# Kernel optimization log

Hardware: AMD Instinct MI355X
Metric: run time of the kernel (lower is better)

The kernel has to match this reference:

```python
import jax, jax.numpy as jnp
import numpy as np

B, L = 16, 54            # dialogues, utterances per dialogue
NDIM = 512; H = 512; NS = 2
T = B * L                # 864 utterances
N = 3 * T                # 2592 nodes (l,a,v per utterance)
NE = B * (L + 3)         # 912 hyperedges (3 modality + L utterance per dialogue)
NNZ = 6 * T              # 5184 incidence entries
E = B * 3 * L * (L - 1)  # 137376 directed intra-modality edges
NUM_L = 3; NUM_K = 4
EPS = 1e-8


def _build_indices():
    rng = np.random.default_rng(0)
    spk = rng.integers(0, NS, size=(B, L))
    # qmask [L, B, NS] one-hot of speakers (matches torch argmax path)
    qmask = np.eye(NS, dtype=np.float32)[spk].transpose(1, 0, 2)
    ar = np.arange(L)
    i1, i2, ht = [], [], []
    for d in range(B):
        base = d * 3 * L
        nl = base + ar; na = nl + L; nv = nl + 2 * L
        # 3 modality hyperedges then L per-utterance (l,a,v) hyperedges
        i1 += [nl, na, nv, np.stack([nl, na, nv], 1).reshape(-1)]
        eb = d * (L + 3)
        i2 += [np.repeat(eb + np.arange(3), L), np.repeat(eb + 3 + ar, 3)]
        ht += [np.ones(L, np.int64), np.zeros(3, np.int64)]
    hyperedge_index = np.stack([np.concatenate(i1), np.concatenate(i2)]).astype(np.int64)
    hyperedge_type = np.concatenate(ht)
    # full permutation edges within each modality of each dialogue
    s0 = np.repeat(ar, L); d0 = np.tile(ar, L)
    m = s0 != d0; s0, d0 = s0[m], d0[m]
    src, dst, et = [], [], []
    for d in range(B):
        same = (spk[d][s0] == spk[d][d0]).astype(np.int64)
        for mm in range(3):
            off = d * 3 * L + mm * L
            src.append(s0 + off); dst.append(d0 + off); et.append(same)
    edge_index = np.stack([np.concatenate(src), np.concatenate(dst)]).astype(np.int64)
    edge_type = np.concatenate(et)
    return qmask, hyperedge_index, hyperedge_type, edge_index, edge_type


def setup_inputs() -> dict:
    key = jax.random.key(0)
    ks = jax.random.split(key, 16)
    qmask, hei, het, ei, et = _build_indices()
    n = lambda k, s: jax.random.normal(k, s, dtype=jnp.float32)
    inp = {
        'a': n(ks[0], (T, NDIM)), 'v': n(ks[1], (T, NDIM)), 'l': n(ks[2], (T, NDIM)),
        'qmask': jnp.asarray(qmask),
        'spk_emb': n(ks[3], (NS, NDIM)) * 0.05,
        'fc1_W': n(ks[4], (NDIM, H)) * 0.05, 'fc1_b': jnp.zeros((H,), jnp.float32),
        'he_weight': jnp.ones((NE,), jnp.float32),
        'ew_weight': jnp.ones((NNZ,), jnp.float32),
        'he_attr1': jax.random.uniform(ks[5], (H,), dtype=jnp.float32),
        'he_attr2': jax.random.uniform(ks[6], (H,), dtype=jnp.float32),
        'hc_W': n(ks[7], (NUM_L, H, H)) * 0.05, 'hc_b': jnp.zeros((NUM_L, H), jnp.float32),
        'm3_W0': n(ks[8], (NUM_K, H, H)) * 0.05,
        'm3_W1': n(ks[9], (NUM_K, H, H)) * 0.05,
        'm3_Wself': n(ks[10], (NUM_K, H, H)) * 0.05,
        'm3_b': jnp.zeros((NUM_K, H), jnp.float32),
        'hyperedge_index': jnp.asarray(hei), 'hyperedge_type': jnp.asarray(het),
        'edge_index': jnp.asarray(ei), 'edge_type': jnp.asarray(et),
    }
    return inp


def reference(a, v, l, qmask, spk_emb, fc1_W, fc1_b, he_weight, ew_weight,
              he_attr1, he_attr2, hc_W, hc_b, m3_W0, m3_W1, m3_Wself, m3_b,
              hyperedge_index, hyperedge_type, edge_index, edge_type):
    seg = jax.ops.segment_sum
    # speaker embedding added to text modality (equal dia_len -> simple transpose)
    qm = qmask.transpose(1, 0, 2).reshape(T, NS)
    l = l + spk_emb[jnp.argmax(qm, axis=-1)]
    # per-dialogue node order: [l_d ; a_d ; v_d]
    feats = jnp.concatenate([l.reshape(B, L, NDIM), a.reshape(B, L, NDIM),
                             v.reshape(B, L, NDIM)], axis=1).reshape(N, NDIM)
    x1 = feats @ fc1_W + fc1_b
    node_i, edge_i = hyperedge_index[0], hyperedge_index[1]
    tfl = hyperedge_type.astype(x1.dtype)[:, None]
    edge_attr = he_attr1[None, :] * tfl + he_attr2[None, :] * (1.0 - tfl)  # [NE,H]
    out = x1
    for ll in range(NUM_L):  # hypergraph conv: gather->edge agg->scatter->linear
        de = seg(ew_weight, edge_i, num_segments=NE)
        e = seg(ew_weight[:, None] * out[node_i], edge_i, num_segments=NE)
        e = e / (de + EPS)[:, None] + edge_attr
        c = he_weight[edge_i]
        dn = seg(c, node_i, num_segments=N)
        agg = seg(c[:, None] * e[edge_i], node_i, num_segments=N) / (dn + EPS)[:, None]
        out = jax.nn.relu(agg @ hc_W[ll] + hc_b[ll])
    src, dst = edge_index[0], edge_index[1]
    same_spk = (edge_type == 1)[:, None]
    deg = seg(jnp.ones_like(dst, dtype=x1.dtype), dst, num_segments=N)
    gnn_out = x1
    denoise = jnp.float32(0.0)
    for kk in range(NUM_K):  # 2-relation RGCN-style denoise layer
        h0 = gnn_out @ m3_W0[kk]
        h1 = gnn_out @ m3_W1[kk]
        msg = jnp.where(same_spk, h1[src], h0[src])
        agg = seg(msg, dst, num_segments=N) / (deg + EPS)[:, None]
        f = jax.nn.relu(agg + gnn_out @ m3_Wself[kk] + m3_b[kk])
        denoise = jnp.mean(f * f)
        gnn_out = gnn_out + f
    return out + gnn_out, denoise
```

## Files before the change

### kernel.cpp

```cpp
#include <hip/hip_runtime.h>

typedef unsigned short ushort_t;
typedef __attribute__((ext_vector_type(4))) float f32x4;
typedef __attribute__((ext_vector_type(8))) short s16x8;
typedef __attribute__((ext_vector_type(8))) unsigned short u16x8;

#define NB 16
#define NL 54
#define NT (NB*NL)
#define NNODE (3*NT)
#define NEDGE 912
#define MATSZ (512*512)

__device__ __forceinline__ ushort_t f2b(float f){
  union {unsigned int i; float f;} x; x.f = f;
  unsigned int r = (x.i + 0x7fffu + ((x.i>>16)&1u))>>16;
  return (ushort_t)r;
}

__device__ __forceinline__ void async_copy16(const ushort_t* g, ushort_t* l){
  __builtin_amdgcn_global_load_lds((const __attribute__((address_space(1))) void*)g,
                                   (__attribute__((address_space(3))) void*)l, 16, 0, 0);
}

__global__ __launch_bounds__(256) void transpose_weights(
    const float* __restrict__ fc1, const float* __restrict__ hc,
    const float* __restrict__ m0, const float* __restrict__ m1,
    const float* __restrict__ ms, ushort_t* __restrict__ WT,
    float* __restrict__ acc, unsigned int* __restrict__ counter)
{
  if (blockIdx.x==0 && blockIdx.y==0 && blockIdx.z==0 && threadIdx.x==0){
    *acc = 0.0f; *counter = 0u;
  }
  int w = blockIdx.z;
  const float* src = (w==0) ? fc1
                   : (w<4)  ? hc + (size_t)(w-1)*MATSZ
                   : (w<8)  ? m0 + (size_t)(w-4)*MATSZ
                   : (w<12) ? m1 + (size_t)(w-8)*MATSZ
                            : ms + (size_t)(w-12)*MATSZ;
  ushort_t* dst = WT + (size_t)w*MATSZ;
  __shared__ float tile[64][65];
  int r0 = blockIdx.x*64, c0 = blockIdx.y*64;
  #pragma unroll
  for (int j=0;j<16;j++){
    int idx = j*256 + threadIdx.x;
    int r = idx>>6, c = idx&63;
    tile[r][c] = src[(size_t)(r0+r)*512 + c0 + c];
  }
  __syncthreads();
  #pragma unroll
  for (int j=0;j<16;j++){
    int idx = j*256 + threadIdx.x;
    int r = idx>>6, c = idx&63;
    dst[(size_t)(c0+r)*512 + r0 + c] = f2b(tile[c][r]);
  }
}

template<int AMODE, bool RELU>
__global__ __launch_bounds__(256) void gemm_kernel(
    const float* __restrict__ Afp, const float* __restrict__ Ebuf,
    const float* __restrict__ inA, const float* __restrict__ inV,
    const float* __restrict__ inL, const float* __restrict__ qmask,
    const float* __restrict__ spk_emb, const float* __restrict__ he_w,
    const ushort_t* __restrict__ WT, const float* __restrict__ bias,
    float* __restrict__ C0, float* __restrict__ C1, float* __restrict__ C2,
    int layer)
{
  const int tid = threadIdx.x;
  const int wave = tid>>6, lane = tid&63;
  const int ml = lane&15, quad = lane>>4;
  const int wr = wave>>1, wc = wave&1;
  int row0 = blockIdx.x*64, col0 = blockIdx.y*128;
  int M = NNODE, cst = 512, cbase = 0;
  const ushort_t* Wsel = WT; float* Cout = C0; const float* bsel = bias;
  const float* Asrc = Afp;
  if (AMODE==2){
    int z = blockIdx.z;
    if (z==0){ Wsel = WT + (size_t)(8+layer)*MATSZ; Cout = C0; bsel = nullptr; }
    else if (z==1){ Wsel = WT + (size_t)(12+layer)*MATSZ; Cout = C1; bsel = bias + layer*512; }
    else {
      if (blockIdx.x >= 4) return;
      int colh = blockIdx.x & 1;
      row0 = (blockIdx.x>>1)*64;
      Wsel = WT + (size_t)(4 + colh*4 + layer)*MATSZ;
      Cout = C2; bsel = nullptr; M = 96; cst = 1024; cbase = colh*512;
      Asrc = Ebuf;
    }
  }

  __shared__ __align__(16) ushort_t As[64][80];
  __shared__ __align__(16) ushort_t Bs[128*64];

  const int ar = tid>>3, ac8 = (tid&7)*8;
  const float *sr0=nullptr,*sr1=nullptr,*sp0=nullptr,*sp1=nullptr;
  const float *e10=nullptr,*e20=nullptr,*e11=nullptr,*e21=nullptr;
  float c10=0.f,c20=0.f,c11=0.f,c21=0.f;
  const float *g0=nullptr,*g1=nullptr;
  {
    int n0 = row0+ar;     if (n0 > M-1) n0 = M-1;
    int n1 = row0+ar+32;  if (n1 > M-1) n1 = M-1;
    if (AMODE==0){
      int d=n0/162, rm=n0-d*162, m=rm/54, i=rm-m*54, t=d*54+i;
      sr0 = ((m==0)? inL : (m==1)? inA : inV) + (size_t)t*512;
      if (m==0) sp0 = spk_emb + ((qmask[(i*16+d)*2+1]>qmask[(i*16+d)*2])?512:0);
      d=n1/162; rm=n1-d*162; m=rm/54; i=rm-m*54; t=d*54+i;
      sr1 = ((m==0)? inL : (m==1)? inA : inV) + (size_t)t*512;
      if (m==0) sp1 = spk_emb + ((qmask[(i*16+d)*2+1]>qmask[(i*16+d)*2])?512:0);
    } else if (AMODE==1){
      int d=n0/162, rm=n0-d*162, m=rm/54, i=rm-m*54;
      int em=d*57+m, eu=d*57+3+i;
      float w1=he_w[em], w2=he_w[eu], inv=1.0f/(w1+w2+1e-8f);
      c10=w1*inv; c20=w2*inv; e10=Ebuf+(size_t)em*512; e20=Ebuf+(size_t)eu*512;
      d=n1/162; rm=n1-d*162; m=rm/54; i=rm-m*54;
      em=d*57+m; eu=d*57+3+i;
      w1=he_w[em]; w2=he_w[eu]; inv=1.0f/(w1+w2+1e-8f);
      c11=w1*inv; c21=w2*inv; e11=Ebuf+(size_t)em*512; e21=Ebuf+(size_t)eu*512;
    } else {
      g0 = Asrc + (size_t)n0*512;
      g1 = Asrc + (size_t)n1*512;
    }
  }

  f32x4 acc[2][4];
  #pragma unroll
  for (int mi=0;mi<2;mi++)
    #pragma unroll
    for (int j=0;j<4;j++) acc[mi][j] = (f32x4){0.f,0.f,0.f,0.f};

  const int lr = lane>>3;
  const int lchunk = lane&7;
  const int bswz = (lchunk ^ lr)*8;

  for (int kk=0; kk<512; kk+=64){
    u16x8 av0, av1;
    if (AMODE==0){
      f32x4 xa=*(const f32x4*)(sr0+kk+ac8), xb=*(const f32x4*)(sr0+kk+ac8+4);
      if (sp0){
        f32x4 sa=*(const f32x4*)(sp0+kk+ac8), sb=*(const f32x4*)(sp0+kk+ac8+4);
        #pragma unroll
        for(int j=0;j<4;j++){ xa[j]+=sa[j]; xb[j]+=sb[j]; }
      }
      #pragma unroll
      for(int j=0;j<4;j++){ av0[j]=f2b(xa[j]); av0[4+j]=f2b(xb[j]); }
      xa=*(const f32x4*)(sr1+kk+ac8); xb=*(const f32x4*)(sr1+kk+ac8+4);
      if (sp1){
        f32x4 sa=*(const f32x4*)(sp1+kk+ac8), sb=*(const f32x4*)(sp1+kk+ac8+4);
        #pragma unroll
        for(int j=0;j<4;j++){ xa[j]+=sa[j]; xb[j]+=sb[j]; }
      }
      #pragma unroll
      for(int j=0;j<4;j++){ av1[j]=f2b(xa[j]); av1[4+j]=f2b(xb[j]); }
    } else if (AMODE==1){
      f32x4 xa=*(const f32x4*)(e10+kk+ac8), xb=*(const f32x4*)(e10+kk+ac8+4);
      f32x4 ya=*(const f32x4*)(e20+kk+ac8), yb=*(const f32x4*)(e20+kk+ac8+4);
      #pragma unroll
      for(int j=0;j<4;j++){ av0[j]=f2b(c10*xa[j]+c20*ya[j]); av0[4+j]=f2b(c10*xb[j]+c20*yb[j]); }
      xa=*(const f32x4*)(e11+kk+ac8); xb=*(const f32x4*)(e11+kk+ac8+4);
      ya=*(const f32x4*)(e21+kk+ac8); yb=*(const f32x4*)(e21+kk+ac8+4);
      #pragma unroll
      for(int j=0;j<4;j++){ av1[j]=f2b(c11*xa[j]+c21*ya[j]); av1[4+j]=f2b(c11*xb[j]+c21*yb[j]); }
    } else {
      f32x4 xa=*(const f32x4*)(g0+kk+ac8), xb=*(const f32x4*)(g0+kk+ac8+4);
      #pragma unroll
      for(int j=0;j<4;j++){ av0[j]=f2b(xa[j]); av0[4+j]=f2b(xb[j]); }
      xa=*(const f32x4*)(g1+kk+ac8); xb=*(const f32x4*)(g1+kk+ac8+4);
      #pragma unroll
      for(int j=0;j<4;j++){ av1[j]=f2b(xa[j]); av1[4+j]=f2b(xb[j]); }
    }
    *(u16x8*)&As[ar][ac8]    = av0;
    *(u16x8*)&As[ar+32][ac8] = av1;

    #pragma unroll
    for (int rep=0; rep<4; rep++){
      int bn0 = wave*32 + rep*8;
      const ushort_t* src = Wsel + (size_t)(col0 + bn0 + lr)*512 + kk + bswz;
      async_copy16(src, &Bs[bn0*64]);
    }
    __syncthreads();

    #pragma unroll
    for (int kh=0; kh<2; kh++){
      s16x8 a0 = *(const s16x8*)&As[wr*32 + ml][kh*32 + quad*8];
      s16x8 a1 = *(const s16x8*)&As[wr*32 + 16 + ml][kh*32 + quad*8];
      s16x8 b[4];
      #pragma unroll
      for (int j=0;j<4;j++){
        int bn = wc*64 + j*16 + ml;
        b[j] = *(const s16x8*)&Bs[bn*64 + (((kh*4+quad) ^ (bn&7))<<3)];
      }
      #pragma unroll
      for (int j=0;j<4;j++){
        acc[0][j] = __builtin_amdgcn_mfma_f32_16x16x32_bf16(a0,b[j],acc[0][j],0,0,0);
        acc[1][j] = __builtin_amdgcn_mfma_f32_16x16x32_bf16(a1,b[j],acc[1][j],0,0,0);
      }
    }
    __syncthreads();
  }

  #pragma unroll
  for (int j=0;j<4;j++){
    int wcol = col0 + wc*64 + j*16 + ml;
    float bv = bsel ? bsel[wcol] : 0.f;
    int c = cbase + wcol;
    #pragma unroll
    for (int mi=0;mi<2;mi++){
      int rb = row0 + wr*32 + mi*16 + quad*4;
      f32x4 a = acc[mi][j];
      #pragma unroll
      for (int r=0;r<4;r++){
        int rr = rb + r;
        if (rr < M){
          float v = a[r] + bv;
          if (RELU) v = fmaxf(v, 0.f);
          Cout[(size_t)rr*cst + c] = v;
        }
      }
    }
  }
}

__global__ __launch_bounds__(256) void edge_kernel(const float* __restrict__ X,
    const float* __restrict__ ew, const int* __restrict__ het,
    const float* __restrict__ at1, const float* __restrict__ at2,
    float* __restrict__ E)
{
  int e = blockIdx.x;
  int d = e/57, r = e - d*57;
  int col = threadIdx.x*2;
  float sx=0.f, sy=0.f, de=0.f;
  if (r < 3){
    int nnz0 = d*324 + r*54;
    const float* row = X + ((size_t)(d*162 + r*54))*512 + col;
    for (int i=0;i<54;i++){
      float w = ew[nnz0+i];
      float2 x = *(const float2*)row;
      sx += w*x.x; sy += w*x.y; de += w;
      row += 512;
    }
  } else {
    int i = r-3;
    int nnz0 = d*324 + 162 + i*3;
    #pragma unroll
    for (int m=0;m<3;m++){
      float w = ew[nnz0+m];
      const float* row = X + ((size_t)(d*162 + m*54 + i))*512 + col;
      float2 x = *(const float2*)row;
      sx += w*x.x; sy += w*x.y; de += w;
    }
  }
  float invde = 1.0f/(de + 1e-8f);
  const float* at = het[e] ? at1 : at2;
  float2 o;
  o.x = sx*invde + at[col];
  o.y = sy*invde + at[col+1];
  *(float2*)(E + (size_t)e*512 + col) = o;
}

__global__ __launch_bounds__(256) void gsum_kernel(const float* __restrict__ X,
    const float* __restrict__ qmask, float* __restrict__ Gsum)
{
  int g = blockIdx.x, d = g/3;
  int col = blockIdx.y*256 + threadIdx.x;
  __shared__ unsigned char spks[54];
  if (threadIdx.x < 54){
    int i = threadIdx.x;
    spks[i] = qmask[(i*16+d)*2+1] > qmask[(i*16+d)*2];
  }
  __syncthreads();
  size_t base = (size_t)g*54*512 + col;
  float s0=0.f, s1=0.f;
  for (int i=0;i<54;i++){
    float x = X[base + (size_t)i*512];
    if (spks[i]) s1 += x; else s0 += x;
  }
  Gsum[(size_t)(g*2)*512 + col]   = s0;
  Gsum[(size_t)(g*2+1)*512 + col] = s1;
}

template<bool LAST>
__global__ __launch_bounds__(256) void sf_kernel(
    const float* __restrict__ Gin, const float* __restrict__ H1,
    const float* __restrict__ HS, const float* __restrict__ Sp,
    const float* __restrict__ qmask, float* __restrict__ Gout,
    float* __restrict__ Gsum, const float* __restrict__ OUThg,
    float* __restrict__ dout, float* __restrict__ acc,
    unsigned int* __restrict__ counter)
{
  int g = blockIdx.x, d = g/3;
  int col = blockIdx.y*256 + threadIdx.x;
  __shared__ unsigned char spks[54];
  if (threadIdx.x < 54){
    int i = threadIdx.x;
    spks[i] = qmask[(i*16+d)*2+1] > qmask[(i*16+d)*2];
  }
  __syncthreads();
  const float* r0 = Sp + (size_t)(g*2)*1024;
  const float* r1 = Sp + (size_t)(g*2+1)*1024;
  float S1_0 = r0[512+col];
  float S1_1 = r1[512+col];
  float S0_0 = r1[col];
  float S0_1 = r0[col];
  const float inv = 1.0f/(53.0f + 1e-8f);
  size_t base = (size_t)g*54*512 + col;
  float gs0=0.f, gs1=0.f, sumsq=0.f;
  for (int i=0;i<54;i++){
    size_t off = base + (size_t)i*512;
    int sp = spks[i];
    float S1 = sp ? S1_1 : S1_0;
    float S0 = sp ? S0_1 : S0_0;
    float h1 = H1[off], hs = HS[off], gi = Gin[off];
    float f = fmaxf((S1 - h1 + S0)*inv + hs, 0.f);
    float gn = gi + f;
    Gout[off] = gn;
    if (sp) gs1 += gn; else gs0 += gn;
    if (LAST){
      sumsq += f*f;
      dout[off] = OUThg[off] + gn;
    }
  }
  Gsum[(size_t)(g*2)*512 + col]   = gs0;
  Gsum[(size_t)(g*2+1)*512 + col] = gs1;
  if (LAST){
    __shared__ float red[256];
    red[threadIdx.x] = sumsq;
    __syncthreads();
    #pragma unroll
    for (int s=128; s>0; s>>=1){
      if (threadIdx.x < s) red[threadIdx.x] += red[threadIdx.x+s];
      __syncthreads();
    }
    if (threadIdx.x == 0){
      atomicAdd(acc, red[0]);
      __threadfence();
      unsigned int old = atomicAdd(counter, 1u);
      if (old == 95u){
        float tot = atomicAdd(acc, 0.0f);
        dout[(size_t)NNODE*512] = tot * (1.0f/1327104.0f);
      }
    }
  }
}

extern "C" void kernel_launch(void* const* d_in, const int* in_sizes, int n_in,
                              void* d_out, int out_size, void* d_ws, size_t ws_size,
                              hipStream_t stream)
{
  const float* A_in   = (const float*)d_in[0];
  const float* V_in   = (const float*)d_in[1];
  const float* L_in   = (const float*)d_in[2];
  const float* qmask  = (const float*)d_in[3];
  const float* spk    = (const float*)d_in[4];
  const float* fc1_W  = (const float*)d_in[5];
  const float* fc1_b  = (const float*)d_in[6];
  const float* he_w   = (const float*)d_in[7];
  const float* ew_w   = (const float*)d_in[8];
  const float* attr1  = (const float*)d_in[9];
  const float* attr2  = (const float*)d_in[10];
  const float* hc_W   = (const float*)d_in[11];
  const float* hc_b   = (const float*)d_in[12];
  const float* m3_W0  = (const float*)d_in[13];
  const float* m3_W1  = (const float*)d_in[14];
  const float* m3_Ws  = (const float*)d_in[15];
  const float* m3_b   = (const float*)d_in[16];
  const int*   het    = (const int*)d_in[18];
  float* dout = (float*)d_out;

  char* ws = (char*)d_ws;
  ushort_t* WT = (ushort_t*)ws;
  float* X1   = (float*)(ws + (size_t)16*MATSZ*2);
  float* OUT  = X1  + (size_t)NNODE*512;
  float* H1   = OUT + (size_t)NNODE*512;
  float* HS   = H1  + (size_t)NNODE*512;
  float* G    = HS  + (size_t)NNODE*512;
  float* EB   = G   + (size_t)NNODE*512;
  float* Gsum = EB  + (size_t)NEDGE*512;
  float* Sp   = Gsum + 96*512;
  float* acc  = Sp  + 96*1024;
  unsigned int* counter = (unsigned int*)(acc + 1);

  transpose_weights<<<dim3(8,8,16),256,0,stream>>>(fc1_W, hc_W, m3_W0, m3_W1,
                                                   m3_Ws, WT, acc, counter);

  gemm_kernel<0,false><<<dim3(41,4,1),256,0,stream>>>(
      nullptr, nullptr, A_in, V_in, L_in, qmask, spk, nullptr,
      WT, fc1_b, X1, nullptr, nullptr, 0);

  gsum_kernel<<<dim3(48,2),256,0,stream>>>(X1, qmask, Gsum);

  const float* src = X1;
  for (int ll=0; ll<3; ll++){
    edge_kernel<<<NEDGE,256,0,stream>>>(src, ew_w, het, attr1, attr2, EB);
    gemm_kernel<1,true><<<dim3(41,4,1),256,0,stream>>>(
        nullptr, EB, nullptr, nullptr, nullptr, nullptr, nullptr, he_w,
        WT + (size_t)(1+ll)*MATSZ, hc_b + (size_t)ll*512, OUT, nullptr, nullptr, 0);
    src = OUT;
  }

  for (int kk=0; kk<4; kk++){
    const float* gin = (kk==0) ? X1 : G;
    gemm_kernel<2,false><<<dim3(41,4,3),256,0,stream>>>(
        gin, Gsum, nullptr, nullptr, nullptr, nullptr, nullptr, nullptr,
        WT, m3_b, H1, HS, Sp, kk);
    if (kk<3)
      sf_kernel<false><<<dim3(48,2),256,0,stream>>>(
          gin, H1, HS, Sp, qmask, G, Gsum, nullptr, nullptr, acc, counter);
    else
      sf_kernel<true><<<dim3(48,2),256,0,stream>>>(
          gin, H1, HS, Sp, qmask, G, Gsum, OUT, dout, acc, counter);
  }

  (void)in_sizes; (void)n_in; (void)out_size; (void)ws_size;
}
```

Measured before the change: 311.3 us.

## Fuse hypergraph and RGCN layers into paired multi-role kernels with folded weights

Restructures the pipeline into alternating ka/kb kernels. Each launch runs the hypergraph edge aggregation, its GEMM, the self/speaker-sum GEMMs and the RGCN update side by side in separate block ranges, which cuts the launch count from about 15 to 10. The per-node h1 term is removed algebraically by folding -W1/53 into the self weight during preprocessing, so the H1 GEMM disappears. The GEMM now stages a full 32x512 A tile in LDS and reads B directly from global memory rather than through an async LDS copy. In exchange it relies on the fixed all-pairs edge structure, uses ping-pong buffers, and bf16 rounding of the folded weights may shift numerics slightly.

```diff
diff --git a/kernel.cpp b/kernel.cpp
--- a/kernel.cpp
+++ b/kernel.cpp
@@ -5,12 +5,9 @@
 typedef __attribute__((ext_vector_type(8))) short s16x8;
 typedef __attribute__((ext_vector_type(8))) unsigned short u16x8;
 
-#define NB 16
-#define NL 54
-#define NT (NB*NL)
-#define NNODE (3*NT)
-#define NEDGE 912
+#define NNODE 2592
 #define MATSZ (512*512)
+#define INV53 (1.0f/(53.0f + 1e-8f))
 
 __device__ __forceinline__ ushort_t f2b(float f){
   union {unsigned int i; float f;} x; x.f = f;
@@ -18,34 +15,31 @@
   return (ushort_t)r;
 }
 
-__device__ __forceinline__ void async_copy16(const ushort_t* g, ushort_t* l){
-  __builtin_amdgcn_global_load_lds((const __attribute__((address_space(1))) void*)g,
-                                   (__attribute__((address_space(3))) void*)l, 16, 0, 0);
-}
-
-__global__ __launch_bounds__(256) void transpose_weights(
+__global__ __launch_bounds__(256) void prep_kernel(
     const float* __restrict__ fc1, const float* __restrict__ hc,
     const float* __restrict__ m0, const float* __restrict__ m1,
     const float* __restrict__ ms, ushort_t* __restrict__ WT,
     float* __restrict__ acc, unsigned int* __restrict__ counter)
 {
-  if (blockIdx.x==0 && blockIdx.y==0 && blockIdx.z==0 && threadIdx.x==0){
-    *acc = 0.0f; *counter = 0u;
-  }
-  int w = blockIdx.z;
+  if (blockIdx.x==0 && threadIdx.x==0){ *acc = 0.f; *counter = 0u; }
+  __shared__ float tile[64][65];
+  int w = blockIdx.x>>6, t = blockIdx.x&63, bx = t>>3, by = t&7;
   const float* src = (w==0) ? fc1
                    : (w<4)  ? hc + (size_t)(w-1)*MATSZ
                    : (w<8)  ? m0 + (size_t)(w-4)*MATSZ
                    : (w<12) ? m1 + (size_t)(w-8)*MATSZ
                             : ms + (size_t)(w-12)*MATSZ;
+  const float* src2 = (w>=12) ? m1 + (size_t)(w-12)*MATSZ : nullptr;
   ushort_t* dst = WT + (size_t)w*MATSZ;
-  __shared__ float tile[64][65];
-  int r0 = blockIdx.x*64, c0 = blockIdx.y*64;
+  int r0 = bx*64, c0 = by*64;
   #pragma unroll
   for (int j=0;j<16;j++){
     int idx = j*256 + threadIdx.x;
     int r = idx>>6, c = idx&63;
-    tile[r][c] = src[(size_t)(r0+r)*512 + c0 + c];
+    size_t off = (size_t)(r0+r)*512 + c0 + c;
+    float v = src[off];
+    if (w>=12) v -= INV53 * src2[off];
+    tile[r][c] = v;
   }
   __syncthreads();
   #pragma unroll
@@ -56,286 +50,330 @@
   }
 }
 
-template<int AMODE, bool RELU>
-__global__ __launch_bounds__(256) void gemm_kernel(
-    const float* __restrict__ Afp, const float* __restrict__ Ebuf,
-    const float* __restrict__ inA, const float* __restrict__ inV,
-    const float* __restrict__ inL, const float* __restrict__ qmask,
-    const float* __restrict__ spk_emb, const float* __restrict__ he_w,
-    const ushort_t* __restrict__ WT, const float* __restrict__ bias,
-    float* __restrict__ C0, float* __restrict__ C1, float* __restrict__ C2,
-    int layer)
+__device__ __forceinline__ void gemm32(const ushort_t* As,
+    const ushort_t* W, int col0, f32x4 acc[2][2])
 {
   const int tid = threadIdx.x;
   const int wave = tid>>6, lane = tid&63;
   const int ml = lane&15, quad = lane>>4;
-  const int wr = wave>>1, wc = wave&1;
-  int row0 = blockIdx.x*64, col0 = blockIdx.y*128;
-  int M = NNODE, cst = 512, cbase = 0;
-  const ushort_t* Wsel = WT; float* Cout = C0; const float* bsel = bias;
-  const float* Asrc = Afp;
-  if (AMODE==2){
-    int z = blockIdx.z;
-    if (z==0){ Wsel = WT + (size_t)(8+layer)*MATSZ; Cout = C0; bsel = nullptr; }
-    else if (z==1){ Wsel = WT + (size_t)(12+layer)*MATSZ; Cout = C1; bsel = bias + layer*512; }
-    else {
-      if (blockIdx.x >= 4) return;
-      int colh = blockIdx.x & 1;
-      row0 = (blockIdx.x>>1)*64;
-      Wsel = WT + (size_t)(4 + colh*4 + layer)*MATSZ;
-      Cout = C2; bsel = nullptr; M = 96; cst = 1024; cbase = colh*512;
-      Asrc = Ebuf;
-    }
-  }
-
-  __shared__ __align__(16) ushort_t As[64][80];
-  __shared__ __align__(16) ushort_t Bs[128*64];
-
-  const int ar = tid>>3, ac8 = (tid&7)*8;
-  const float *sr0=nullptr,*sr1=nullptr,*sp0=nullptr,*sp1=nullptr;
-  const float *e10=nullptr,*e20=nullptr,*e11=nullptr,*e21=nullptr;
-  float c10=0.f,c20=0.f,c11=0.f,c21=0.f;
-  const float *g0=nullptr,*g1=nullptr;
+  #pragma unroll
+  for (int mf=0;mf<2;mf++)
+    #pragma unroll
+    for (int nf=0;nf<2;nf++) acc[mf][nf] = (f32x4){0.f,0.f,0.f,0.f};
+
+  const ushort_t* bw0 = W + (size_t)(col0 + wave*32 + ml)*512 + quad*8;
+  const ushort_t* bw1 = bw0 + (size_t)16*512;
+  const int rsw = ml&7;
+  #pragma unroll
+  for (int ks=0; ks<16; ks++){
+    const int chunk = ks*4 + quad;
+    const int abase = (chunk>>3)*64 + (((chunk&7) ^ rsw)<<3);
+    s16x8 a0 = *(const s16x8*)&As[(size_t)ml*512 + abase];
+    s16x8 a1 = *(const s16x8*)&As[(size_t)(16+ml)*512 + abase];
+    s16x8 b0 = *(const s16x8*)(bw0 + ks*32);
+    s16x8 b1 = *(const s16x8*)(bw1 + ks*32);
+    acc[0][0] = __builtin_amdgcn_mfma_f32_16x16x32_bf16(a0,b0,acc[0][0],0,0,0);
+    acc[0][1] = __builtin_amdgcn_mfma_f32_16x16x32_bf16(a0,b1,acc[0][1],0,0,0);
+    acc[1][0] = __builtin_amdgcn_mfma_f32_16x16x32_bf16(a1,b0,acc[1][0],0,0,0);
+    acc[1][1] = __builtin_amdgcn_mfma_f32_16x16x32_bf16(a1,b1,acc[1][1],0,0,0);
+  }
+}
+
+__global__ __launch_bounds__(256) void fc1_kernel(
+    const float* __restrict__ A_in, const float* __restrict__ V_in,
+    const float* __restrict__ L_in, const float* __restrict__ qmask,
+    const float* __restrict__ spk, const ushort_t* __restrict__ WT,
+    const float* __restrict__ fc1_b, float* __restrict__ X1)
+{
+  __shared__ __align__(16) ushort_t As[32*512];
+  const int b = blockIdx.x, tid = threadIdx.x;
+  const int r0 = (b>>2)*32, col0 = (b&3)*128;
   {
-    int n0 = row0+ar;     if (n0 > M-1) n0 = M-1;
-    int n1 = row0+ar+32;  if (n1 > M-1) n1 = M-1;
-    if (AMODE==0){
-      int d=n0/162, rm=n0-d*162, m=rm/54, i=rm-m*54, t=d*54+i;
-      sr0 = ((m==0)? inL : (m==1)? inA : inV) + (size_t)t*512;
-      if (m==0) sp0 = spk_emb + ((qmask[(i*16+d)*2+1]>qmask[(i*16+d)*2])?512:0);
-      d=n1/162; rm=n1-d*162; m=rm/54; i=rm-m*54; t=d*54+i;
-      sr1 = ((m==0)? inL : (m==1)? inA : inV) + (size_t)t*512;
-      if (m==0) sp1 = spk_emb + ((qmask[(i*16+d)*2+1]>qmask[(i*16+d)*2])?512:0);
-    } else if (AMODE==1){
-      int d=n0/162, rm=n0-d*162, m=rm/54, i=rm-m*54;
-      int em=d*57+m, eu=d*57+3+i;
-      float w1=he_w[em], w2=he_w[eu], inv=1.0f/(w1+w2+1e-8f);
-      c10=w1*inv; c20=w2*inv; e10=Ebuf+(size_t)em*512; e20=Ebuf+(size_t)eu*512;
-      d=n1/162; rm=n1-d*162; m=rm/54; i=rm-m*54;
-      em=d*57+m; eu=d*57+3+i;
-      w1=he_w[em]; w2=he_w[eu]; inv=1.0f/(w1+w2+1e-8f);
-      c11=w1*inv; c21=w2*inv; e11=Ebuf+(size_t)em*512; e21=Ebuf+(size_t)eu*512;
+    int row = tid>>3, seg = tid&7, gr = r0+row;
+    int d = gr/162, rm = gr-d*162, m = rm/54, i = rm-m*54, t = d*54+i;
+    const float* pa = ((m==0)?L_in:(m==1)?A_in:V_in) + (size_t)t*512 + seg*64;
+    const float* pb = pa;
+    bool hassp = (m==0);
+    if (hassp){
+      int sp = qmask[(i*16+d)*2+1] > qmask[(i*16+d)*2];
+      pb = spk + sp*512 + seg*64;
+    }
+    int rsw = row&7;
+    ushort_t* dstA = &As[row*512 + seg*64];
+    #pragma unroll
+    for (int j=0;j<8;j++){
+      f32x4 xa = *(const f32x4*)(pa+j*8), xb = *(const f32x4*)(pa+j*8+4);
+      if (hassp){
+        f32x4 ya = *(const f32x4*)(pb+j*8), yb = *(const f32x4*)(pb+j*8+4);
+        #pragma unroll
+        for (int jj=0;jj<4;jj++){ xa[jj]+=ya[jj]; xb[jj]+=yb[jj]; }
+      }
+      u16x8 v;
+      #pragma unroll
+      for (int jj=0;jj<4;jj++){ v[jj]=f2b(xa[jj]); v[4+jj]=f2b(xb[jj]); }
+      *(u16x8*)&dstA[(j ^ rsw)<<3] = v;
+    }
+  }
+  __syncthreads();
+  f32x4 acc[2][2];
+  gemm32(As, WT, col0, acc);
+  const int wave = tid>>6, lane = tid&63;
+  const int ml = lane&15, quad = lane>>4;
+  #pragma unroll
+  for (int nf=0;nf<2;nf++){
+    int col = col0 + wave*32 + nf*16 + ml;
+    float bv = fc1_b[col];
+    #pragma unroll
+    for (int mf=0;mf<2;mf++)
+      #pragma unroll
+      for (int r=0;r<4;r++){
+        int gr = r0 + mf*16 + quad*4 + r;
+        X1[(size_t)gr*512 + col] = acc[mf][nf][r] + bv;
+      }
+  }
+}
+
+__global__ __launch_bounds__(256) void ka_kernel(int kk,
+    const float* __restrict__ gin, const float* __restrict__ GsIn,
+    const ushort_t* __restrict__ WT, const float* __restrict__ m3_b,
+    float* __restrict__ HS, float* __restrict__ Sp,
+    const float* __restrict__ qmask,
+    const float* __restrict__ edge_src, const float* __restrict__ ew_w,
+    const int* __restrict__ het, const float* __restrict__ attr1,
+    const float* __restrict__ attr2, float* __restrict__ EB)
+{
+  __shared__ __align__(16) union {
+    ushort_t As[32*512];
+    struct { float gsum[6][512]; unsigned char spks[54]; } sp;
+  } sm;
+  const int b = blockIdx.x, tid = threadIdx.x;
+  if (b < 324){
+    const int r0 = (b>>2)*32, col0 = (b&3)*128;
+    {
+      int row = tid>>3, seg = tid&7;
+      const float* p = gin + (size_t)(r0+row)*512 + seg*64;
+      int rsw = row&7;
+      ushort_t* dstA = &sm.As[row*512 + seg*64];
+      #pragma unroll
+      for (int j=0;j<8;j++){
+        f32x4 xa = *(const f32x4*)(p+j*8), xb = *(const f32x4*)(p+j*8+4);
+        u16x8 v;
+        #pragma unroll
+        for (int jj=0;jj<4;jj++){ v[jj]=f2b(xa[jj]); v[4+jj]=f2b(xb[jj]); }
+        *(u16x8*)&dstA[(j ^ rsw)<<3] = v;
+      }
+    }
+    __syncthreads();
+    f32x4 acc[2][2];
+    gemm32(sm.As, WT + (size_t)(12+kk)*MATSZ, col0, acc);
+    const int wave = tid>>6, lane = tid&63;
+    const int ml = lane&15, quad = lane>>4;
+    #pragma unroll
+    for (int nf=0;nf<2;nf++){
+      int col = col0 + wave*32 + nf*16 + ml;
+      float bv = m3_b[kk*512 + col];
+      #pragma unroll
+      for (int mf=0;mf<2;mf++)
+        #pragma unroll
+        for (int r=0;r<4;r++){
+          int gr = r0 + mf*16 + quad*4 + r;
+          HS[(size_t)gr*512 + col] = acc[mf][nf][r] + bv;
+        }
+    }
+  } else if (b < 340){
+    const int d = b - 324;
+    if (kk == 0){
+      if (tid < 54)
+        sm.sp.spks[tid] = qmask[(tid*16+d)*2+1] > qmask[(tid*16+d)*2];
+      __syncthreads();
+      int c = tid*2;
+      #pragma unroll
+      for (int m=0;m<3;m++){
+        float a0=0.f,b0v=0.f,a1=0.f,b1v=0.f;
+        for (int i=0;i<54;i++){
+          float2 x = *(const float2*)&gin[(size_t)(d*162+m*54+i)*512 + c];
+          if (sm.sp.spks[i]){ a1+=x.x; b1v+=x.y; } else { a0+=x.x; b0v+=x.y; }
+        }
+        sm.sp.gsum[m*2][c]   = a0;  sm.sp.gsum[m*2][c+1]   = b0v;
+        sm.sp.gsum[m*2+1][c] = a1;  sm.sp.gsum[m*2+1][c+1] = b1v;
+      }
     } else {
-      g0 = Asrc + (size_t)n0*512;
-      g1 = Asrc + (size_t)n1*512;
-    }
-  }
-
-  f32x4 acc[2][4];
-  #pragma unroll
-  for (int mi=0;mi<2;mi++)
-    #pragma unroll
-    for (int j=0;j<4;j++) acc[mi][j] = (f32x4){0.f,0.f,0.f,0.f};
-
-  const int lr = lane>>3;
-  const int lchunk = lane&7;
-  const int bswz = (lchunk ^ lr)*8;
-
-  for (int kk=0; kk<512; kk+=64){
-    u16x8 av0, av1;
-    if (AMODE==0){
-      f32x4 xa=*(const f32x4*)(sr0+kk+ac8), xb=*(const f32x4*)(sr0+kk+ac8+4);
-      if (sp0){
-        f32x4 sa=*(const f32x4*)(sp0+kk+ac8), sb=*(const f32x4*)(sp0+kk+ac8+4);
-        #pragma unroll
-        for(int j=0;j<4;j++){ xa[j]+=sa[j]; xb[j]+=sb[j]; }
-      }
-      #pragma unroll
-      for(int j=0;j<4;j++){ av0[j]=f2b(xa[j]); av0[4+j]=f2b(xb[j]); }
-      xa=*(const f32x4*)(sr1+kk+ac8); xb=*(const f32x4*)(sr1+kk+ac8+4);
-      if (sp1){
-        f32x4 sa=*(const f32x4*)(sp1+kk+ac8), sb=*(const f32x4*)(sp1+kk+ac8+4);
-        #pragma unroll
-        for(int j=0;j<4;j++){ xa[j]+=sa[j]; xb[j]+=sb[j]; }
-      }
-      #pragma unroll
-      for(int j=0;j<4;j++){ av1[j]=f2b(xa[j]); av1[4+j]=f2b(xb[j]); }
-    } else if (AMODE==1){
-      f32x4 xa=*(const f32x4*)(e10+kk+ac8), xb=*(const f32x4*)(e10+kk+ac8+4);
-      f32x4 ya=*(const f32x4*)(e20+kk+ac8), yb=*(const f32x4*)(e20+kk+ac8+4);
-      #pragma unroll
-      for(int j=0;j<4;j++){ av0[j]=f2b(c10*xa[j]+c20*ya[j]); av0[4+j]=f2b(c10*xb[j]+c20*yb[j]); }
-      xa=*(const f32x4*)(e11+kk+ac8); xb=*(const f32x4*)(e11+kk+ac8+4);
-      ya=*(const f32x4*)(e21+kk+ac8); yb=*(const f32x4*)(e21+kk+ac8+4);
-      #pragma unroll
-      for(int j=0;j<4;j++){ av1[j]=f2b(c11*xa[j]+c21*ya[j]); av1[4+j]=f2b(c11*xb[j]+c21*yb[j]); }
+      const f32x4* g4 = (const f32x4*)(GsIn + (size_t)d*6*512);
+      f32x4* l4 = (f32x4*)sm.sp.gsum;
+      for (int idx=tid; idx<768; idx+=256) l4[idx] = g4[idx];
+    }
+    __syncthreads();
+    const int wave = tid>>6, lane = tid&63;
+    const int ml = lane&15, quad = lane>>4;
+    const ushort_t* Wb = WT + (size_t)((wave<2 ? 4 : 8)+kk)*MATSZ;
+    const int colbase = (wave&1)*256;
+    f32x4 sac[16];
+    #pragma unroll
+    for (int nf=0;nf<16;nf++) sac[nf] = (f32x4){0.f,0.f,0.f,0.f};
+    for (int ks=0; ks<16; ks++){
+      u16x8 af;
+      if (ml < 6){
+        const float* gr = &sm.sp.gsum[ml][ks*32 + quad*8];
+        f32x4 xa = *(const f32x4*)gr, xb = *(const f32x4*)(gr+4);
+        #pragma unroll
+        for (int j=0;j<4;j++){ af[j]=f2b(xa[j]); af[4+j]=f2b(xb[j]); }
+      } else af = (u16x8){0,0,0,0,0,0,0,0};
+      #pragma unroll
+      for (int nf=0; nf<16; nf++){
+        const ushort_t* wp = Wb + (size_t)(colbase + nf*16 + ml)*512 + ks*32 + quad*8;
+        s16x8 bf = *(const s16x8*)wp;
+        sac[nf] = __builtin_amdgcn_mfma_f32_16x16x32_bf16((s16x8)af, bf, sac[nf],0,0,0);
+      }
+    }
+    #pragma unroll
+    for (int nf=0; nf<16; nf++){
+      #pragma unroll
+      for (int r=0;r<4;r++){
+        int row = quad*4 + r;
+        if (row < 6)
+          Sp[(size_t)(d*6+row)*1024 + wave*256 + nf*16 + ml] = sac[nf][r];
+      }
+    }
+  } else {
+    int e = b - 340;
+    int d = e/57, r = e - d*57;
+    int col = tid*2;
+    float sx=0.f, sy=0.f, de=0.f;
+    if (r < 3){
+      int nnz0 = d*324 + r*54;
+      const float* row = edge_src + ((size_t)(d*162 + r*54))*512 + col;
+      for (int i=0;i<54;i++){
+        float w = ew_w[nnz0+i];
+        float2 x = *(const float2*)row;
+        sx += w*x.x; sy += w*x.y; de += w;
+        row += 512;
+      }
     } else {
-      f32x4 xa=*(const f32x4*)(g0+kk+ac8), xb=*(const f32x4*)(g0+kk+ac8+4);
-      #pragma unroll
-      for(int j=0;j<4;j++){ av0[j]=f2b(xa[j]); av0[4+j]=f2b(xb[j]); }
-      xa=*(const f32x4*)(g1+kk+ac8); xb=*(const f32x4*)(g1+kk+ac8+4);
-      #pragma unroll
-      for(int j=0;j<4;j++){ av1[j]=f2b(xa[j]); av1[4+j]=f2b(xb[j]); }
-    }
-    *(u16x8*)&As[ar][ac8]    = av0;
-    *(u16x8*)&As[ar+32][ac8] = av1;
-
-    #pragma unroll
-    for (int rep=0; rep<4; rep++){
-      int bn0 = wave*32 + rep*8;
-      const ushort_t* src = Wsel + (size_t)(col0 + bn0 + lr)*512 + kk + bswz;
-      async_copy16(src, &Bs[bn0*64]);
+      int i = r-3;
+      int nnz0 = d*324 + 162 + i*3;
+      #pragma unroll
+      for (int m=0;m<3;m++){
+        float w = ew_w[nnz0+m];
+        const float* row = edge_src + ((size_t)(d*162 + m*54 + i))*512 + col;
+        float2 x = *(const float2*)row;
+        sx += w*x.x; sy += w*x.y; de += w;
+      }
+    }
+    float invde = 1.0f/(de + 1e-8f);
+    const float* at = het[e] ? attr1 : attr2;
+    float2 o;
+    o.x = sx*invde + at[col];
+    o.y = sy*invde + at[col+1];
+    *(float2*)(EB + (size_t)e*512 + col) = o;
+  }
+}
+
+template<bool LAST>
+__global__ __launch_bounds__(256) void kb_kernel(int lk,
+    const float* __restrict__ EB, const ushort_t* __restrict__ WT,
+    const float* __restrict__ hc_b, float* __restrict__ dst,
+    const float* __restrict__ gin, const float* __restrict__ HS,
+    const float* __restrict__ Sp, const float* __restrict__ qmask,
+    const float* __restrict__ he_w,
+    float* __restrict__ Gout, float* __restrict__ GsOut,
+    const float* __restrict__ OUThg, float* __restrict__ dout,
+    float* __restrict__ accp, unsigned int* __restrict__ counter)
+{
+  __shared__ __align__(16) union {
+    ushort_t As[32*512];
+    struct { unsigned char spks[54]; float red[256]; } sf;
+  } sm;
+  const int b = blockIdx.x, tid = threadIdx.x;
+  if (!LAST && b < 324){
+    const int r0 = (b>>2)*32, col0 = (b&3)*128;
+    {
+      int row = tid>>3, seg = tid&7, gr = r0+row;
+      int d = gr/162, rm = gr-d*162, m = rm/54, i = rm-m*54;
+      int em = d*57+m, eu = d*57+3+i;
+      float w1 = he_w[em], w2 = he_w[eu], inv = 1.0f/(w1+w2+1e-8f);
+      float c1 = w1*inv, c2 = w2*inv;
+      const float* pa = EB + (size_t)em*512 + seg*64;
+      const float* pb = EB + (size_t)eu*512 + seg*64;
+      int rsw = row&7;
+      ushort_t* dstA = &sm.As[row*512 + seg*64];
+      #pragma unroll
+      for (int j=0;j<8;j++){
+        f32x4 xa = *(const f32x4*)(pa+j*8), xb = *(const f32x4*)(pa+j*8+4);
+        f32x4 ya = *(const f32x4*)(pb+j*8), yb = *(const f32x4*)(pb+j*8+4);
+        u16x8 v;
+        #pragma unroll
+        for (int jj=0;jj<4;jj++){
+          v[jj]   = f2b(c1*xa[jj] + c2*ya[jj]);
+          v[4+jj] = f2b(c1*xb[jj] + c2*yb[jj]);
+        }
+        *(u16x8*)&dstA[(j ^ rsw)<<3] = v;
+      }
     }
     __syncthreads();
-
-    #pragma unroll
-    for (int kh=0; kh<2; kh++){
-      s16x8 a0 = *(const s16x8*)&As[wr*32 + ml][kh*32 + quad*8];
-      s16x8 a1 = *(const s16x8*)&As[wr*32 + 16 + ml][kh*32 + quad*8];
-      s16x8 b[4];
-      #pragma unroll
-      for (int j=0;j<4;j++){
-        int bn = wc*64 + j*16 + ml;
-        b[j] = *(const s16x8*)&Bs[bn*64 + (((kh*4+quad) ^ (bn&7))<<3)];
-      }
-      #pragma unroll
-      for (int j=0;j<4;j++){
-        acc[0][j] = __builtin_amdgcn_mfma_f32_16x16x32_bf16(a0,b[j],acc[0][j],0,0,0);
-        acc[1][j] = __builtin_amdgcn_mfma_f32_16x16x32_bf16(a1,b[j],acc[1][j],0,0,0);
-      }
-    }
+    f32x4 acc[2][2];
+    gemm32(sm.As, WT + (size_t)(1+lk)*MATSZ, col0, acc);
+    const int wave = tid>>6, lane = tid&63;
+    const int ml = lane&15, quad = lane>>4;
+    #pragma unroll
+    for (int nf=0;nf<2;nf++){
+      int col = col0 + wave*32 + nf*16 + ml;
+      float bv = hc_b[lk*512 + col];
+      #pragma unroll
+      for (int mf=0;mf<2;mf++)
+        #pragma unroll
+        for (int r=0;r<4;r++){
+          int gr = r0 + mf*16 + quad*4 + r;
+          dst[(size_t)gr*512 + col] = fmaxf(acc[mf][nf][r] + bv, 0.f);
+        }
+    }
+  } else {
+    const int sfid = LAST ? b : b-324;
+    const int g = sfid>>1, d = g/3;
+    const int col = (sfid&1)*256 + tid;
+    if (tid < 54)
+      sm.sf.spks[tid] = qmask[(tid*16+d)*2+1] > qmask[(tid*16+d)*2];
     __syncthreads();
-  }
-
-  #pragma unroll
-  for (int j=0;j<4;j++){
-    int wcol = col0 + wc*64 + j*16 + ml;
-    float bv = bsel ? bsel[wcol] : 0.f;
-    int c = cbase + wcol;
-    #pragma unroll
-    for (int mi=0;mi<2;mi++){
-      int rb = row0 + wr*32 + mi*16 + quad*4;
-      f32x4 a = acc[mi][j];
-      #pragma unroll
-      for (int r=0;r<4;r++){
-        int rr = rb + r;
-        if (rr < M){
-          float v = a[r] + bv;
-          if (RELU) v = fmaxf(v, 0.f);
-          Cout[(size_t)rr*cst + c] = v;
-        }
-      }
-    }
-  }
-}
-
-__global__ __launch_bounds__(256) void edge_kernel(const float* __restrict__ X,
-    const float* __restrict__ ew, const int* __restrict__ het,
-    const float* __restrict__ at1, const float* __restrict__ at2,
-    float* __restrict__ E)
-{
-  int e = blockIdx.x;
-  int d = e/57, r = e - d*57;
-  int col = threadIdx.x*2;
-  float sx=0.f, sy=0.f, de=0.f;
-  if (r < 3){
-    int nnz0 = d*324 + r*54;
-    const float* row = X + ((size_t)(d*162 + r*54))*512 + col;
+    const float* r0p = Sp + (size_t)(g*2)*1024;
+    const float* r1p = Sp + (size_t)(g*2+1)*1024;
+    float S1_0 = r0p[512+col];
+    float S1_1 = r1p[512+col];
+    float S0_0 = r1p[col];
+    float S0_1 = r0p[col];
+    size_t base = (size_t)g*54*512 + col;
+    float gs0=0.f, gs1=0.f, sumsq=0.f;
     for (int i=0;i<54;i++){
-      float w = ew[nnz0+i];
-      float2 x = *(const float2*)row;
-      sx += w*x.x; sy += w*x.y; de += w;
-      row += 512;
-    }
-  } else {
-    int i = r-3;
-    int nnz0 = d*324 + 162 + i*3;
-    #pragma unroll
-    for (int m=0;m<3;m++){
-      float w = ew[nnz0+m];
-      const float* row = X + ((size_t)(d*162 + m*54 + i))*512 + col;
-      float2 x = *(const float2*)row;
-      sx += w*x.x; sy += w*x.y; de += w;
-    }
-  }
-  float invde = 1.0f/(de + 1e-8f);
-  const float* at = het[e] ? at1 : at2;
-  float2 o;
-  o.x = sx*invde + at[col];
-  o.y = sy*invde + at[col+1];
-  *(float2*)(E + (size_t)e*512 + col) = o;
-}
-
-__global__ __launch_bounds__(256) void gsum_kernel(const float* __restrict__ X,
-    const float* __restrict__ qmask, float* __restrict__ Gsum)
-{
-  int g = blockIdx.x, d = g/3;
-  int col = blockIdx.y*256 + threadIdx.x;
-  __shared__ unsigned char spks[54];
-  if (threadIdx.x < 54){
-    int i = threadIdx.x;
-    spks[i] = qmask[(i*16+d)*2+1] > qmask[(i*16+d)*2];
-  }
-  __syncthreads();
-  size_t base = (size_t)g*54*512 + col;
-  float s0=0.f, s1=0.f;
-  for (int i=0;i<54;i++){
-    float x = X[base + (size_t)i*512];
-    if (spks[i]) s1 += x; else s0 += x;
-  }
-  Gsum[(size_t)(g*2)*512 + col]   = s0;
-  Gsum[(size_t)(g*2+1)*512 + col] = s1;
-}
-
-template<bool LAST>
-__global__ __launch_bounds__(256) void sf_kernel(
-    const float* __restrict__ Gin, const float* __restrict__ H1,
-    const float* __restrict__ HS, const float* __restrict__ Sp,
-    const float* __restrict__ qmask, float* __restrict__ Gout,
-    float* __restrict__ Gsum, const float* __restrict__ OUThg,
-    float* __restrict__ dout, float* __restrict__ acc,
-    unsigned int* __restrict__ counter)
-{
-  int g = blockIdx.x, d = g/3;
-  int col = blockIdx.y*256 + threadIdx.x;
-  __shared__ unsigned char spks[54];
-  if (threadIdx.x < 54){
-    int i = threadIdx.x;
-    spks[i] = qmask[(i*16+d)*2+1] > qmask[(i*16+d)*2];
-  }
-  __syncthreads();
-  const float* r0 = Sp + (size_t)(g*2)*1024;
-  const float* r1 = Sp + (size_t)(g*2+1)*1024;
-  float S1_0 = r0[512+col];
-  float S1_1 = r1[512+col];
-  float S0_0 = r1[col];
-  float S0_1 = r0[col];
-  const float inv = 1.0f/(53.0f + 1e-8f);
-  size_t base = (size_t)g*54*512 + col;
-  float gs0=0.f, gs1=0.f, sumsq=0.f;
-  for (int i=0;i<54;i++){
-    size_t off = base + (size_t)i*512;
-    int sp = spks[i];
-    float S1 = sp ? S1_1 : S1_0;
-    float S0 = sp ? S0_1 : S0_0;
-    float h1 = H1[off], hs = HS[off], gi = Gin[off];
-    float f = fmaxf((S1 - h1 + S0)*inv + hs, 0.f);
-    float gn = gi + f;
-    Gout[off] = gn;
-    if (sp) gs1 += gn; else gs0 += gn;
-    if (LAST){
-      sumsq += f*f;
-      dout[off] = OUThg[off] + gn;
-    }
-  }
-  Gsum[(size_t)(g*2)*512 + col]   = gs0;
-  Gsum[(size_t)(g*2+1)*512 + col] = gs1;
-  if (LAST){
-    __shared__ float red[256];
-    red[threadIdx.x] = sumsq;
-    __syncthreads();
-    #pragma unroll
-    for (int s=128; s>0; s>>=1){
-      if (threadIdx.x < s) red[threadIdx.x] += red[threadIdx.x+s];
+      size_t off = base + (size_t)i*512;
+      int sp = sm.sf.spks[i];
+      float S1 = sp ? S1_1 : S1_0;
+      float S0 = sp ? S0_1 : S0_0;
+      float hs = HS[off], gi = gin[off];
+      float f = fmaxf((S1 + S0)*INV53 + hs, 0.f);
+      float gn = gi + f;
+      if (LAST){
+        sumsq += f*f;
+        dout[off] = OUThg[off] + gn;
+      } else {
+        Gout[off] = gn;
+        if (sp) gs1 += gn; else gs0 += gn;
+      }
+    }
+    if (!LAST){
+      GsOut[(size_t)(g*2)*512 + col]   = gs0;
+      GsOut[(size_t)(g*2+1)*512 + col] = gs1;
+    } else {
+      sm.sf.red[tid] = sumsq;
       __syncthreads();
-    }
-    if (threadIdx.x == 0){
-      atomicAdd(acc, red[0]);
-      __threadfence();
-      unsigned int old = atomicAdd(counter, 1u);
-      if (old == 95u){
-        float tot = atomicAdd(acc, 0.0f);
-        dout[(size_t)NNODE*512] = tot * (1.0f/1327104.0f);
+      #pragma unroll
+      for (int s=128; s>0; s>>=1){
+        if (tid < s) sm.sf.red[tid] += sm.sf.red[tid+s];
+        __syncthreads();
+      }
+      if (tid == 0){
+        atomicAdd(accp, sm.sf.red[0]);
+        __threadfence();
+        unsigned int old = atomicAdd(counter, 1u);
+        if (old == 95u)
+          dout[(size_t)NNODE*512] = atomicAdd(accp, 0.0f) * (1.0f/1327104.0f);
       }
     }
   }
@@ -367,47 +405,40 @@
 
   char* ws = (char*)d_ws;
   ushort_t* WT = (ushort_t*)ws;
-  float* X1   = (float*)(ws + (size_t)16*MATSZ*2);
-  float* OUT  = X1  + (size_t)NNODE*512;
-  float* H1   = OUT + (size_t)NNODE*512;
-  float* HS   = H1  + (size_t)NNODE*512;
-  float* G    = HS  + (size_t)NNODE*512;
-  float* EB   = G   + (size_t)NNODE*512;
-  float* Gsum = EB  + (size_t)NEDGE*512;
-  float* Sp   = Gsum + 96*512;
-  float* acc  = Sp  + 96*1024;
+  float* X1 = (float*)(ws + (size_t)16*MATSZ*2);
+  float* OA = X1 + (size_t)NNODE*512;
+  float* OB = OA + (size_t)NNODE*512;
+  float* OC = OB + (size_t)NNODE*512;
+  float* GA = OC + (size_t)NNODE*512;
+  float* GB = GA + (size_t)NNODE*512;
+  float* HS = GB + (size_t)NNODE*512;
+  float* EB = HS + (size_t)NNODE*512;
+  float* Sp = EB + (size_t)912*512;
+  float* GsA = Sp + 96*1024;
+  float* GsB = GsA + 96*512;
+  float* acc = GsB + 96*512;
   unsigned int* counter = (unsigned int*)(acc + 1);
 
-  transpose_weights<<<dim3(8,8,16),256,0,stream>>>(fc1_W, hc_W, m3_W0, m3_W1,
-                                                   m3_Ws, WT, acc, counter);
-
-  gemm_kernel<0,false><<<dim3(41,4,1),256,0,stream>>>(
-      nullptr, nullptr, A_in, V_in, L_in, qmask, spk, nullptr,
-      WT, fc1_b, X1, nullptr, nullptr, 0);
-
-  gsum_kernel<<<dim3(48,2),256,0,stream>>>(X1, qmask, Gsum);
-
-  const float* src = X1;
-  for (int ll=0; ll<3; ll++){
-    edge_kernel<<<NEDGE,256,0,stream>>>(src, ew_w, het, attr1, attr2, EB);
-    gemm_kernel<1,true><<<dim3(41,4,1),256,0,stream>>>(
-        nullptr, EB, nullptr, nullptr, nullptr, nullptr, nullptr, he_w,
-        WT + (size_t)(1+ll)*MATSZ, hc_b + (size_t)ll*512, OUT, nullptr, nullptr, 0);
-    src = OUT;
-  }
-
-  for (int kk=0; kk<4; kk++){
-    const float* gin = (kk==0) ? X1 : G;
-    gemm_kernel<2,false><<<dim3(41,4,3),256,0,stream>>>(
-        gin, Gsum, nullptr, nullptr, nullptr, nullptr, nullptr, nullptr,
-        WT, m3_b, H1, HS, Sp, kk);
-    if (kk<3)
-      sf_kernel<false><<<dim3(48,2),256,0,stream>>>(
-          gin, H1, HS, Sp, qmask, G, Gsum, nullptr, nullptr, acc, counter);
-    else
-      sf_kernel<true><<<dim3(48,2),256,0,stream>>>(
-          gin, H1, HS, Sp, qmask, G, Gsum, OUT, dout, acc, counter);
-  }
+  prep_kernel<<<1024,256,0,stream>>>(fc1_W, hc_W, m3_W0, m3_W1, m3_Ws,
+                                     WT, acc, counter);
+  fc1_kernel<<<324,256,0,stream>>>(A_in, V_in, L_in, qmask, spk, WT, fc1_b, X1);
+
+  ka_kernel<<<1252,256,0,stream>>>(0, X1, GsA, WT, m3_b, HS, Sp, qmask,
+                                   X1, ew_w, het, attr1, attr2, EB);
+  kb_kernel<false><<<420,256,0,stream>>>(0, EB, WT, hc_b, OA, X1, HS, Sp,
+      qmask, he_w, GA, GsA, nullptr, nullptr, acc, counter);
+  ka_kernel<<<1252,256,0,stream>>>(1, GA, GsA, WT, m3_b, HS, Sp, qmask,
+                                   OA, ew_w, het, attr1, attr2, EB);
+  kb_kernel<false><<<420,256,0,stream>>>(1, EB, WT, hc_b, OB, GA, HS, Sp,
+      qmask, he_w, GB, GsB, nullptr, nullptr, acc, counter);
+  ka_kernel<<<1252,256,0,stream>>>(2, GB, GsB, WT, m3_b, HS, Sp, qmask,
+                                   OB, ew_w, het, attr1, attr2, EB);
+  kb_kernel<false><<<420,256,0,stream>>>(2, EB, WT, hc_b, OC, GB, HS, Sp,
+      qmask, he_w, GA, GsA, nullptr, nullptr, acc, counter);
+  ka_kernel<<<340,256,0,stream>>>(3, GA, GsA, WT, m3_b, HS, Sp, qmask,
+                                  nullptr, ew_w, het, attr1, attr2, EB);
+  kb_kernel<true><<<96,256,0,stream>>>(3, EB, WT, hc_b, nullptr, GA, HS, Sp,
+      qmask, he_w, nullptr, nullptr, OC, dout, acc, counter);
 
   (void)in_sizes; (void)n_in; (void)out_size; (void)ws_size;
 }
```

Result: slower. 466.5 us (+49.9%).
